# Kernel tuning notes

Measured on AMD Instinct MI355X. Metric: run time of the kernel, lower is better.

The kernel has to match this reference:

```python
import jax, jax.numpy as jnp
import numpy as np

B, T, H = 8, 1024, 640
N_PHONE, N_PHONEME = 230, 96


def _make_mapping():
    # 0/1 phone->phoneme allophone map, shape (n_phoneme, n_phone).
    # Every phone maps to >=1 phoneme; every phoneme covered (n_phone > n_phoneme).
    rng = np.random.default_rng(0)
    m = np.zeros((N_PHONEME, N_PHONE), dtype=np.float32)
    cols = np.arange(N_PHONE)
    m[cols % N_PHONEME, cols] = 1.0
    m[rng.integers(0, N_PHONEME, size=N_PHONE), cols] = 1.0  # some phones are allophones of 2 phonemes
    m[0, 0] = 1.0  # blank -> blank, as in allophone_layer
    return jnp.asarray(m)


def setup_inputs() -> dict:
    key = jax.random.key(0)
    k1, k2 = jax.random.split(key)
    enc_output = jax.random.normal(k1, (B, T, H), dtype=jnp.float32)
    feature2phone = jax.random.normal(k2, (H, N_PHONE), dtype=jnp.float32)
    return {"enc_output": enc_output, "feature2phone": feature2phone, "mapping": _make_mapping()}


def reference(enc_output, feature2phone, mapping):
    # phone logits: (B,T,H) @ (H,P) -> (B,T,P), scaled by sqrt(H)
    hidden = feature2phone.shape[0]
    phone = jnp.einsum('bth,hp->btp', enc_output, feature2phone) / jnp.sqrt(jnp.asarray(hidden, enc_output.dtype))
    # broadcast-multiply with 0/1 map -> (B,T,M,P), mask zeros with -inf
    allo = phone[:, :, None, :] * mapping  # mapping: (M,P)
    allo = jnp.where(mapping > 0, allo, -jnp.inf)
    # masked max segment-reduce over the phone axis -> (B,T,M)
    phoneme = jnp.max(allo, axis=-1)
    # log-softmax over phoneme dim
    return jax.nn.log_softmax(phoneme, axis=2)
```

## Files before the change

### kernel.cpp

```cpp
#include <hip/hip_runtime.h>
#include <math.h>

#define NH 640
#define NP 230
#define NM 96
#define NROWS 8192
#define MAXL 32
#define NSTEP 20
#define MBLK 32
#define NBLOCKS (NROWS / MBLK)

#define OFF_CNT  0
#define OFF_CSR  4096
#define OFF_B    65536

typedef __bf16 bf16_t;
typedef bf16_t bf16x8 __attribute__((ext_vector_type(8)));
typedef float floatx4 __attribute__((ext_vector_type(4)));

static __device__ __forceinline__ unsigned short f2b(float f) {
    unsigned u = __float_as_uint(f);
    u += 0x7fffu + ((u >> 16) & 1u);
    return (unsigned short)(u >> 16);
}

__global__ __launch_bounds__(256)
void prep_kernel(const float* __restrict__ f2p,
                 const float* __restrict__ mapping,
                 int* __restrict__ cnt, int* __restrict__ csr,
                 unsigned short* __restrict__ wsB2) {
    const int b = blockIdx.x;
    const int tid = threadIdx.x;
    if (b < 24) {
        int wave = b * 4 + (tid >> 6);
        int lane = tid & 63;
        if (wave >= NM) return;
        int base = 0;
        #pragma unroll
        for (int c = 0; c < 4; ++c) {
            int p = c * 64 + lane;
            float v = (p < NP) ? mapping[wave * NP + p] : 0.0f;
            unsigned long long mask = __ballot(v > 0.0f);
            if (v > 0.0f) {
                int idx = base + __popcll(mask & ((1ull << lane) - 1ull));
                if (idx < MAXL) csr[wave * MAXL + idx] = p;
            }
            base += __popcll(mask);
        }
        if (lane == 0) cnt[wave] = base < MAXL ? base : MAXL;
    } else {
        int g = (b - 24) * 256 + tid;
        int m16  = g & 15;
        int quad = (g >> 4) & 3;
        int ct   = (g >> 6) & 15;
        int s    = g >> 10;
        int n = ct * 16 + m16;
        int k0 = s * 32 + quad * 8;
        unsigned short v[8];
        #pragma unroll
        for (int j = 0; j < 8; ++j)
            v[j] = (n < NP) ? f2b(f2p[(size_t)(k0 + j) * NP + n]) : (unsigned short)0;
        *(uint4*)(wsB2 + (size_t)g * 8) = *(const uint4*)v;
    }
}

__global__ __launch_bounds__(512, 1)
void fused_phonetics_kernel(const float* __restrict__ enc,
                            const unsigned short* __restrict__ wsB2,
                            const int* __restrict__ cnt,
                            const int* __restrict__ csr,
                            float* __restrict__ out) {
    __shared__ __align__(16) unsigned short sA[2560 * 8];
    float (*phone)[257] = (float (*)[257])sA;

    const int tid  = threadIdx.x;
    const int lane = tid & 63;
    const int wv   = tid >> 6;
    const int m16  = lane & 15;
    const int quad = lane >> 4;
    const int row0 = blockIdx.x * MBLK;

    #pragma unroll
    for (int i = 0; i < 10; ++i) {
        int F = i * 2048 + tid * 4;
        int row = F / 640;
        int k   = F - row * 640;
        float4 a = *(const float4*)(enc + (size_t)row0 * NH + F);
        int s  = k >> 5;
        int q  = (k & 31) >> 3;
        int j0 = k & 7;
        unsigned short v[4];
        v[0] = f2b(a.x); v[1] = f2b(a.y); v[2] = f2b(a.z); v[3] = f2b(a.w);
        int soff = ((s * 2 + (row >> 4)) * 64 + q * 16 + (row & 15)) * 8 + j0;
        *(uint2*)(sA + soff) = *(const uint2*)v;
    }
    __syncthreads();

    floatx4 acc00 = {0.f,0.f,0.f,0.f}, acc01 = acc00, acc10 = acc00, acc11 = acc00;

    const unsigned short* aptr = sA + (size_t)lane * 8;
    const unsigned short* bptr = wsB2 + ((size_t)(wv * 2) * 64 + lane) * 8;

    #pragma unroll
    for (int s = 0; s < NSTEP; ++s) {
        uint4 a0 = *(const uint4*)(aptr + (size_t)(s * 2 + 0) * 64 * 8);
        uint4 a1 = *(const uint4*)(aptr + (size_t)(s * 2 + 1) * 64 * 8);
        uint4 b0 = *(const uint4*)(bptr + ((size_t)s * 16 + 0) * 64 * 8);
        uint4 b1 = *(const uint4*)(bptr + ((size_t)s * 16 + 1) * 64 * 8);
        bf16x8 A0 = __builtin_bit_cast(bf16x8, a0);
        bf16x8 A1 = __builtin_bit_cast(bf16x8, a1);
        bf16x8 B0 = __builtin_bit_cast(bf16x8, b0);
        bf16x8 B1 = __builtin_bit_cast(bf16x8, b1);
        acc00 = __builtin_amdgcn_mfma_f32_16x16x32_bf16(A0, B0, acc00, 0, 0, 0);
        acc01 = __builtin_amdgcn_mfma_f32_16x16x32_bf16(A0, B1, acc01, 0, 0, 0);
        acc10 = __builtin_amdgcn_mfma_f32_16x16x32_bf16(A1, B0, acc10, 0, 0, 0);
        acc11 = __builtin_amdgcn_mfma_f32_16x16x32_bf16(A1, B1, acc11, 0, 0, 0);
    }

    __syncthreads();

    const float scale = 0.03952847075210474f;
    #pragma unroll
    for (int i = 0; i < 4; ++i) {
        int r = quad * 4 + i;
        phone[r     ][wv * 32 +  0 + m16] = acc00[i] * scale;
        phone[r     ][wv * 32 + 16 + m16] = acc01[i] * scale;
        phone[r + 16][wv * 32 +  0 + m16] = acc10[i] * scale;
        phone[r + 16][wv * 32 + 16 + m16] = acc11[i] * scale;
    }
    __syncthreads();

    const int r   = tid >> 4;
    const int l16 = tid & 15;
    float pmv[6];
    float mx = -INFINITY;
    #pragma unroll
    for (int j = 0; j < 6; ++j) {
        int m = l16 + j * 16;
        int c = cnt[m];
        const int* lst = csr + m * MAXL;
        float best = -INFINITY;
        for (int jj = 0; jj < c; ++jj) best = fmaxf(best, phone[r][lst[jj]]);
        pmv[j] = best;
        mx = fmaxf(mx, best);
    }
    #pragma unroll
    for (int d = 1; d < 16; d <<= 1) mx = fmaxf(mx, __shfl_xor(mx, d));
    float s = 0.f;
    #pragma unroll
    for (int j = 0; j < 6; ++j) s += __expf(pmv[j] - mx);
    #pragma unroll
    for (int d = 1; d < 16; d <<= 1) s += __shfl_xor(s, d);
    const float lse = mx + __logf(s);
    #pragma unroll
    for (int j = 0; j < 6; ++j)
        out[(size_t)(row0 + r) * NM + l16 + j * 16] = pmv[j] - lse;
}

extern "C" void kernel_launch(void* const* d_in, const int* in_sizes, int n_in,
                              void* d_out, int out_size, void* d_ws, size_t ws_size,
                              hipStream_t stream) {
    const float* enc     = (const float*)d_in[0];
    const float* f2p     = (const float*)d_in[1];
    const float* mapping = (const float*)d_in[2];
    float* out = (float*)d_out;

    char* ws = (char*)d_ws;
    int* cnt = (int*)(ws + OFF_CNT);
    int* csr = (int*)(ws + OFF_CSR);
    unsigned short* wsB2 = (unsigned short*)(ws + OFF_B);

    prep_kernel<<<104, 256, 0, stream>>>(f2p, mapping, cnt, csr, wsB2);
    fused_phonetics_kernel<<<NBLOCKS, 512, 0, stream>>>(enc, wsB2, cnt, csr, out);
}
```

Baseline: 85.40 us.

## Prefetch A and early B tiles into registers, stage CSR map in LDS

All global loads of the enc tile and the first eight B k-steps are issued up front into registers, so their latency overlaps rather than serialising with the convert/store and the MFMA loop. The cnt/csr mapping tables are copied into shared memory so the gather phase reads LDS instead of scattered global memory. Launch bounds now allow two blocks per CU. The trade-off is higher register pressure and extra LDS, which may limit how much occupancy is actually gained.

```diff
diff --git a/kernel.cpp b/kernel.cpp
--- a/kernel.cpp
+++ b/kernel.cpp
@@ -9,6 +9,7 @@
 #define NSTEP 20
 #define MBLK 32
 #define NBLOCKS (NROWS / MBLK)
+#define PFB 8
 
 #define OFF_CNT  0
 #define OFF_CSR  4096
@@ -64,13 +65,15 @@
     }
 }
 
-__global__ __launch_bounds__(512, 1)
+__global__ __launch_bounds__(512, 2)
 void fused_phonetics_kernel(const float* __restrict__ enc,
                             const unsigned short* __restrict__ wsB2,
                             const int* __restrict__ cnt,
                             const int* __restrict__ csr,
                             float* __restrict__ out) {
     __shared__ __align__(16) unsigned short sA[2560 * 8];
+    __shared__ int scnt[NM];
+    __shared__ int scsr[NM * MAXL];
     float (*phone)[257] = (float (*)[257])sA;
 
     const int tid  = threadIdx.x;
@@ -80,17 +83,35 @@
     const int quad = lane >> 4;
     const int row0 = blockIdx.x * MBLK;
 
+    float4 areg[10];
+    #pragma unroll
+    for (int i = 0; i < 10; ++i)
+        areg[i] = *(const float4*)(enc + (size_t)row0 * NH + i * 2048 + tid * 4);
+
+    const unsigned short* bptr = wsB2 + ((size_t)(wv * 2) * 64 + lane) * 8;
+    uint4 bpre[2 * PFB];
+    #pragma unroll
+    for (int s = 0; s < PFB; ++s) {
+        bpre[2 * s + 0] = *(const uint4*)(bptr + ((size_t)s * 16 + 0) * 64 * 8);
+        bpre[2 * s + 1] = *(const uint4*)(bptr + ((size_t)s * 16 + 1) * 64 * 8);
+    }
+
+    if (tid < NM) scnt[tid] = cnt[tid];
+    #pragma unroll
+    for (int j = 0; j < 6; ++j)
+        scsr[tid + j * 512] = csr[tid + j * 512];
+
     #pragma unroll
     for (int i = 0; i < 10; ++i) {
         int F = i * 2048 + tid * 4;
         int row = F / 640;
         int k   = F - row * 640;
-        float4 a = *(const float4*)(enc + (size_t)row0 * NH + F);
         int s  = k >> 5;
         int q  = (k & 31) >> 3;
         int j0 = k & 7;
         unsigned short v[4];
-        v[0] = f2b(a.x); v[1] = f2b(a.y); v[2] = f2b(a.z); v[3] = f2b(a.w);
+        v[0] = f2b(areg[i].x); v[1] = f2b(areg[i].y);
+        v[2] = f2b(areg[i].z); v[3] = f2b(areg[i].w);
         int soff = ((s * 2 + (row >> 4)) * 64 + q * 16 + (row & 15)) * 8 + j0;
         *(uint2*)(sA + soff) = *(const uint2*)v;
     }
@@ -99,14 +120,19 @@
     floatx4 acc00 = {0.f,0.f,0.f,0.f}, acc01 = acc00, acc10 = acc00, acc11 = acc00;
 
     const unsigned short* aptr = sA + (size_t)lane * 8;
-    const unsigned short* bptr = wsB2 + ((size_t)(wv * 2) * 64 + lane) * 8;
 
     #pragma unroll
     for (int s = 0; s < NSTEP; ++s) {
         uint4 a0 = *(const uint4*)(aptr + (size_t)(s * 2 + 0) * 64 * 8);
         uint4 a1 = *(const uint4*)(aptr + (size_t)(s * 2 + 1) * 64 * 8);
-        uint4 b0 = *(const uint4*)(bptr + ((size_t)s * 16 + 0) * 64 * 8);
-        uint4 b1 = *(const uint4*)(bptr + ((size_t)s * 16 + 1) * 64 * 8);
+        uint4 b0, b1;
+        if (s < PFB) {
+            b0 = bpre[2 * s + 0];
+            b1 = bpre[2 * s + 1];
+        } else {
+            b0 = *(const uint4*)(bptr + ((size_t)s * 16 + 0) * 64 * 8);
+            b1 = *(const uint4*)(bptr + ((size_t)s * 16 + 1) * 64 * 8);
+        }
         bf16x8 A0 = __builtin_bit_cast(bf16x8, a0);
         bf16x8 A1 = __builtin_bit_cast(bf16x8, a1);
         bf16x8 B0 = __builtin_bit_cast(bf16x8, b0);
@@ -137,8 +163,8 @@
     #pragma unroll
     for (int j = 0; j < 6; ++j) {
         int m = l16 + j * 16;
-        int c = cnt[m];
-        const int* lst = csr + m * MAXL;
+        int c = scnt[m];
+        const int* lst = scsr + m * MAXL;
         float best = -INFINITY;
         for (int jj = 0; jj < c; ++jj) best = fmaxf(best, phone[r][lst[jj]]);
         pmv[j] = best;
```

Result: faster. 82.30 us (-3.6%).
